# Kernel optimization log

Measured on AMD Instinct MI355X. Metric: run time of the kernel, lower is better.

Reference implementation:

```python
import jax, jax.numpy as jnp
import numpy as np

HEADS = 4

def _layernorm(x, g, b, eps=1e-5):
    mu = x.mean(-1, keepdims=True)
    var = ((x - mu) ** 2).mean(-1, keepdims=True)
    return (x - mu) / jnp.sqrt(var + eps) * g + b

def _feature_map(data, proj, is_query, eps=1e-4):
    # FAVOR+ softmax kernel features. data: [B,H,S,dh], proj: [m,dh]
    dh = data.shape[-1]
    m = proj.shape[0]
    dn = dh ** -0.25
    ratio = m ** -0.5
    dash = jnp.einsum('bhsd,md->bhsm', data * dn, proj)
    diag = 0.5 * jnp.sum((data * dn) ** 2, axis=-1, keepdims=True)
    mx = jnp.max(dash, axis=-1, keepdims=True) if is_query else jnp.max(dash)
    return ratio * (jnp.exp(dash - diag - mx) + eps)

def _causal_linear_attention(q, k, v):
    # q,k: [B,H,S,m] kernel features; v: [B,H,S,dh]
    k_cum = jnp.cumsum(k, axis=2)                                  # [B,H,S,m]
    d_inv = 1.0 / jnp.einsum('bhsm,bhsm->bhs', q, k_cum)           # [B,H,S]
    ctx = jnp.cumsum(jnp.einsum('bhsm,bhsd->bhsmd', k, v), axis=2) # [B,H,S,m,dh]
    return jnp.einsum('bhsmd,bhsm,bhs->bhsd', ctx, q, d_inv)

def reference(x, pre_w, pre_b, ln1_g, ln1_b, wq, wk, wv, wo, bo, proj,
              ln2_g, ln2_b, ff_w1, ff_b1, ff_w2, ff_b2, tgt_w, tgt_b, rd_w, rd_b):
    # preproc: 1x1x1 conv3d + softplus
    xbn = jax.nn.softplus(jnp.einsum('bcthw,oc->bothw', x, pre_w)
                          + pre_b[None, :, None, None, None])
    B, D, T, H, W = xbn.shape
    tokens = xbn.reshape(B, -1, D)  # raw torch-style reshape, S = T*H*W
    S = tokens.shape[1]

    # Performer block (depth=1): prenorm attention + prenorm FF, residuals
    h = _layernorm(tokens, ln1_g, ln1_b)
    split = lambda t: t.reshape(B, S, HEADS, -1).transpose(0, 2, 1, 3)
    q, k, v = split(h @ wq), split(h @ wk), split(h @ wv)
    qp = _feature_map(q, proj, True)
    kp = _feature_map(k, proj, False)
    attn = _causal_linear_attention(qp, kp, v)
    attn = attn.transpose(0, 2, 1, 3).reshape(B, S, D)
    tokens = tokens + attn @ wo + bo
    h2 = _layernorm(tokens, ln2_g, ln2_b)
    tokens = tokens + jax.nn.gelu(h2 @ ff_w1 + ff_b1, approximate=False) @ ff_w2 + ff_b2

    # readout
    out = tokens.reshape(B, D, T, H, W).mean(axis=2)               # [B,D,H,W]
    out = jnp.concatenate([out, x[:, 2, 0][:, None]], axis=1)      # [B,D+1,H,W]
    out = jax.lax.conv_general_dilated(out, tgt_w, (1, 1), [(2, 2), (2, 2)],
                                       dimension_numbers=('NCHW', 'OIHW', 'NCHW'))
    out = out + tgt_b[None, :, None, None]
    out = out.mean(axis=(2, 3))                                    # global avg pool -> [B,1]
    return out @ rd_w.T + rd_b


def setup_inputs() -> dict:
    key = jax.random.key(0)
    ks = jax.random.split(key, 12)
    B, T, H, W = 2, 8, 48, 48
    D, DH, M, FF = 64, 16, 32, 256
    s = lambda k, shape, sc=1.0: jax.random.normal(k, shape, jnp.float32) * sc
    inv = 1.0 / np.sqrt(D)
    return {
        'x': s(ks[0], (B, 3, T, H, W)),
        'pre_w': s(ks[1], (D, 3), 1.0 / np.sqrt(3)),
        'pre_b': jnp.zeros((D,), jnp.float32),
        'ln1_g': jnp.ones((D,), jnp.float32), 'ln1_b': jnp.zeros((D,), jnp.float32),
        'wq': s(ks[2], (D, D), inv), 'wk': s(ks[3], (D, D), inv), 'wv': s(ks[4], (D, D), inv),
        'wo': s(ks[5], (D, D), inv), 'bo': jnp.zeros((D,), jnp.float32),
        'proj': s(ks[6], (M, DH)),
        'ln2_g': jnp.ones((D,), jnp.float32), 'ln2_b': jnp.zeros((D,), jnp.float32),
        'ff_w1': s(ks[7], (D, FF), inv), 'ff_b1': jnp.zeros((FF,), jnp.float32),
        'ff_w2': s(ks[8], (FF, D), 1.0 / np.sqrt(FF)), 'ff_b2': jnp.zeros((D,), jnp.float32),
        'tgt_w': s(ks[9], (1, D + 1, 5, 5), 1.0 / np.sqrt((D + 1) * 25)),
        'tgt_b': jnp.zeros((1,), jnp.float32),
        'rd_w': s(ks[10], (1, 1)), 'rd_b': jnp.zeros((1,), jnp.float32),
    }
```

## Files before the change

### kernel.cpp

```cpp
#include <hip/hip_runtime.h>
#include <hip/hip_bf16.h>
#include <math.h>

typedef __hip_bfloat16 bf16;
typedef __attribute__((ext_vector_type(8))) short short8;
typedef __attribute__((ext_vector_type(16))) float floatx16;

constexpr int B_   = 2;
constexpr int T_   = 8;
constexpr int HW   = 48 * 48;
constexpr int S_   = T_ * HW;
constexpr int D_   = 64;
constexpr int NH   = 4;
constexpr int DH   = 16;
constexpr int M_   = 32;
constexpr int BS   = B_ * S_;
constexpr int BSD  = BS * D_;
constexpr int BH   = B_ * NH;
constexpr int BHS  = BH * S_;
constexpr int CHUNK = 32;
constexpr int NC   = S_ / CHUNK;
constexpr int STATE = M_ * DH + M_;
constexpr int GSLOTS = 64;
constexpr int GSTRIDE = 32;
constexpr int SCB = 16;
constexpr int SRG = 16;
constexpr int SRUN = NC / SRG;
constexpr float DN = 0.5f;
constexpr float RATIO = 0.17677669529663687f;

__device__ __forceinline__ unsigned short f2bf(float f) {
  bf16 h = __float2bfloat16(f);
  return *reinterpret_cast<unsigned short*>(&h);
}
__device__ __forceinline__ float bf2f(bf16 v) { return __bfloat162float(v); }
__device__ __forceinline__ float bfs2f(short s) {
  return __uint_as_float(((unsigned)(unsigned short)s) << 16);
}
__device__ __forceinline__ void atomicMaxFloat(float* addr, float val) {
  if (val >= 0.f) atomicMax((int*)addr, __float_as_int(val));
  else atomicMin((unsigned int*)addr, __float_as_uint(val));
}

__global__ void __launch_bounds__(256) k_prep(const float* __restrict__ wq,
        const float* __restrict__ wk, const float* __restrict__ wv,
        const float* __restrict__ wo, const float* __restrict__ w1,
        const float* __restrict__ proj,
        short* __restrict__ wqT, short* __restrict__ wkT, short* __restrict__ wvT,
        short* __restrict__ woT, short* __restrict__ w1T, short* __restrict__ projb,
        float* __restrict__ gmax) {
  int tid = blockIdx.x * 256 + threadIdx.x;
  if (tid < GSLOTS) ((unsigned*)gmax)[tid * GSTRIDE] = 0xff800000u;
  if (tid < 512) projb[tid] = (short)f2bf(proj[tid]);
  if (tid < 4096) {
    int c = tid >> 6, r = tid & 63;
    wqT[tid] = (short)f2bf(wq[r * 64 + c]);
    wkT[tid] = (short)f2bf(wk[r * 64 + c]);
    wvT[tid] = (short)f2bf(wv[r * 64 + c]);
    woT[tid] = (short)f2bf(wo[r * 64 + c]);
  }
  {
    int c = tid >> 6, r = tid & 63;
    w1T[tid] = (short)f2bf(w1[r * 256 + c]);
  }
}

__global__ void __launch_bounds__(256) k_preqkv(const float* __restrict__ x,
                      const float* __restrict__ pw, const float* __restrict__ pb,
                      const float* __restrict__ g, const float* __restrict__ bb,
                      const short* __restrict__ wqT, const short* __restrict__ wkT,
                      const short* __restrict__ wvT, const short* __restrict__ projb,
                      bf16* __restrict__ tok, bf16* __restrict__ q,
                      bf16* __restrict__ k, bf16* __restrict__ v,
                      float* __restrict__ gmax) {
  __shared__ __align__(16) short sh[32 * 64];
  __shared__ __align__(16) short sk[32 * 64];
  int tid = threadIdx.x;
  int tbase = blockIdx.x * 32;

  {
    size_t f0 = (size_t)tbase * 64;
    int b = (int)(f0 / ((size_t)D_ * S_));
    int rem = (int)(f0 % ((size_t)D_ * S_));
    int d = rem / S_;
    int pos0 = rem % S_;
    float w0 = pw[d * 3 + 0], w1 = pw[d * 3 + 1], w2 = pw[d * 3 + 2], pbd = pb[d];
    const float* xb = x + ((size_t)b * 3) * S_ + pos0 + tid * 8;
    float4 x0a = *(const float4*)(xb);
    float4 x0b = *(const float4*)(xb + 4);
    float4 x1a = *(const float4*)(xb + S_);
    float4 x1b = *(const float4*)(xb + S_ + 4);
    float4 x2a = *(const float4*)(xb + 2 * S_);
    float4 x2b = *(const float4*)(xb + 2 * S_ + 4);
    float xf0[8] = {x0a.x, x0a.y, x0a.z, x0a.w, x0b.x, x0b.y, x0b.z, x0b.w};
    float xf1[8] = {x1a.x, x1a.y, x1a.z, x1a.w, x1b.x, x1b.y, x1b.z, x1b.w};
    float xf2[8] = {x2a.x, x2a.y, x2a.z, x2a.w, x2b.x, x2b.y, x2b.z, x2b.w};
    float t[8];
    short8 tv;
#pragma unroll
    for (int j = 0; j < 8; ++j) {
      float a = xf0[j] * w0 + xf1[j] * w1 + xf2[j] * w2 + pbd;
      t[j] = fmaxf(a, 0.f) + log1pf(expf(-fabsf(a)));
      tv[j] = (short)f2bf(t[j]);
    }
    *(short8*)(tok + f0 + (size_t)tid * 8) = tv;
    float s1 = 0.f, s2 = 0.f;
#pragma unroll
    for (int j = 0; j < 8; ++j) { s1 += t[j]; s2 += t[j] * t[j]; }
#pragma unroll
    for (int off = 4; off; off >>= 1) {
      s1 += __shfl_xor(s1, off, 8);
      s2 += __shfl_xor(s2, off, 8);
    }
    float mu = s1 * (1.f / 64.f);
    float var = s2 * (1.f / 64.f) - mu * mu;
    float rs = rsqrtf(var + 1e-5f);
    int tt = tid >> 3, j8 = tid & 7;
    short8 hv;
#pragma unroll
    for (int j = 0; j < 8; ++j) {
      int c = j8 * 8 + j;
      hv[j] = (short)f2bf((t[j] - mu) * rs * g[c] + bb[c]);
    }
    *(short8*)&sh[tt * 64 + ((j8 ^ (tt & 7)) * 8)] = hv;
  }
  __syncthreads();

  int w = tid >> 6;
  int L = tid & 63;
  int half = L >> 5;
  int n = L & 31;

  if (w < 3) {
    const short* wmT = (w == 0) ? wqT : (w == 1) ? wkT : wvT;
    bf16* outm = (w == 0) ? q : (w == 1) ? k : v;

    short8 a[4];
#pragma unroll
    for (int c = 0; c < 4; ++c)
      a[c] = *(const short8*)&sh[n * 64 + (((c * 2 + half) ^ (n & 7)) * 8)];
#pragma unroll
    for (int ct = 0; ct < 2; ++ct) {
      int col = ct * 32 + n;
      short8 bfrag[4];
#pragma unroll
      for (int c = 0; c < 4; ++c)
        bfrag[c] = *(const short8*)&wmT[col * 64 + c * 16 + half * 8];
      floatx16 acc;
#pragma unroll
      for (int i = 0; i < 16; ++i) acc[i] = 0.f;
      acc = __builtin_amdgcn_mfma_f32_32x32x16_bf16(a[0], bfrag[0], acc, 0, 0, 0);
      acc = __builtin_amdgcn_mfma_f32_32x32x16_bf16(a[1], bfrag[1], acc, 0, 0, 0);
      acc = __builtin_amdgcn_mfma_f32_32x32x16_bf16(a[2], bfrag[2], acc, 0, 0, 0);
      acc = __builtin_amdgcn_mfma_f32_32x32x16_bf16(a[3], bfrag[3], acc, 0, 0, 0);
      int head = col >> 4, di = col & 15;
#pragma unroll
      for (int r = 0; r < 16; ++r) {
        int row = (r & 3) + 8 * (r >> 2) + 4 * half;
        int token = tbase + row;
        int b = token / S_, s = token % S_;
        unsigned short us = f2bf(acc[r]);
        if (w == 2) {
          outm[((size_t)(b * NH + head) * S_ + s) * DH + di] = *(bf16*)&us;
        } else {
          unsigned short usd = f2bf(bfs2f((short)us) * DN);
          outm[((size_t)(b * NH + head) * S_ + s) * DH + di] = *(bf16*)&usd;
          if (w == 1)
            *(short*)((char*)sk + row * 128 + ((col * 2) ^ ((row & 7) << 4))) = (short)usd;
        }
      }
    }
  }
  __syncthreads();

  {
    short8 ak;
    short8 bp = *(const short8*)&projb[n * 16 + half * 8];
    int roff = n * 128 + ((w * 32 + half * 16) ^ ((n & 7) << 4));
    ak = *(const short8*)((const char*)sk + roff);
    floatx16 Pk;
#pragma unroll
    for (int i = 0; i < 16; ++i) Pk[i] = 0.f;
    Pk = __builtin_amdgcn_mfma_f32_32x32x16_bf16(ak, bp, Pk, 0, 0, 0);
    float bmax = -3.4e38f;
#pragma unroll
    for (int r = 0; r < 16; ++r) bmax = fmaxf(bmax, Pk[r]);
    for (int off = 32; off; off >>= 1) bmax = fmaxf(bmax, __shfl_xor(bmax, off));
    if (L == 0)
      atomicMaxFloat(&gmax[((blockIdx.x * 4 + w) & (GSLOTS - 1)) * GSTRIDE], bmax);
  }
}

__global__ void __launch_bounds__(256) k_featcsfin(const float* __restrict__ gmax,
                      const bf16* __restrict__ q, const bf16* __restrict__ k,
                      const bf16* __restrict__ v, const short* __restrict__ projb,
                      bf16* __restrict__ qpb, bf16* __restrict__ kpb,
                      float* __restrict__ ckv) {
  __shared__ __align__(16) float sKp[CHUNK * 32];
  __shared__ __align__(16) float sVc[CHUNK * 16];
  int tid = threadIdx.x;
  int w = tid >> 6, L = tid & 63, half = L >> 5, n = L & 31;
  short8 bp = *(const short8*)&projb[n * 16 + half * 8];

  if (blockIdx.x >= BH * NC) {
    int fblk = blockIdx.x - BH * NC;
    int rowbase = fblk * 128 + w * 32;
    short8 aq = *(const short8*)(q + (size_t)(rowbase + n) * 16 + half * 8);
    float dq = 0.f;
#pragma unroll
    for (int j = 0; j < 8; ++j) { float f = bfs2f(aq[j]); dq += f * f; }
    dq += __shfl_xor(dq, 32);
    dq *= 0.5f;
    floatx16 Pq;
#pragma unroll
    for (int i = 0; i < 16; ++i) Pq[i] = 0.f;
    Pq = __builtin_amdgcn_mfma_f32_32x32x16_bf16(aq, bp, Pq, 0, 0, 0);
#pragma unroll
    for (int r = 0; r < 16; ++r) {
      int i = (r & 3) + 8 * (r >> 2) + 4 * half;
      float mx = Pq[r];
      for (int off = 16; off; off >>= 1) mx = fmaxf(mx, __shfl_xor(mx, off, 32));
      float dqi = __shfl(dq, i, 64);
      float val = RATIO * (expf(Pq[r] - dqi - mx) + 1e-4f);
      qpb[(size_t)(rowbase + i) * 32 + n] = __float2bfloat16(val);
    }
    return;
  }

  int blk = blockIdx.x;
  int bh = blk / NC, c = blk % NC;
  int base = bh * S_ + c * CHUNK;
  if (w == 0) {
    float gm = gmax[L * GSTRIDE];
    for (int off = 32; off; off >>= 1) gm = fmaxf(gm, __shfl_xor(gm, off));
    short8 ak = *(const short8*)(k + (size_t)(base + n) * 16 + half * 8);
    float dk = 0.f;
#pragma unroll
    for (int j = 0; j < 8; ++j) { float f = bfs2f(ak[j]); dk += f * f; }
    dk += __shfl_xor(dk, 32);
    dk *= 0.5f;
    floatx16 Pk;
#pragma unroll
    for (int i = 0; i < 16; ++i) Pk[i] = 0.f;
    Pk = __builtin_amdgcn_mfma_f32_32x32x16_bf16(ak, bp, Pk, 0, 0, 0);
#pragma unroll
    for (int r = 0; r < 16; ++r) {
      int i = (r & 3) + 8 * (r >> 2) + 4 * half;
      float dgi = __shfl(dk, i, 64);
      sKp[i * 32 + n] = RATIO * (expf(Pk[r] - dgi - gm) + 1e-4f);
    }
  } else if (w == 1) {
    int row = L >> 1, h8 = (L & 1) * 8;
    short8 vs = *(const short8*)(v + (size_t)(base + row) * 16 + h8);
#pragma unroll
    for (int j = 0; j < 8; ++j) sVc[row * 16 + h8 + j] = bfs2f(vs[j]);
  }
  __syncthreads();
  {
    int row = tid >> 3, m4 = tid & 7;
    float4 fin = *(const float4*)&sKp[row * 32 + m4 * 4];
    uint2 u;
    u.x = (unsigned)f2bf(fin.x) | ((unsigned)f2bf(fin.y) << 16);
    u.y = (unsigned)f2bf(fin.z) | ((unsigned)f2bf(fin.w) << 16);
    *(uint2*)&kpb[(size_t)(base + row) * 32 + m4 * 4] = u;
  }
  int m0 = tid >> 4, d0 = tid & 15;
  int m1 = m0 + 16;
  float a0 = 0.f, a1 = 0.f, az0 = 0.f, az1 = 0.f;
  for (int t = 0; t < CHUNK; ++t) {
    float k0 = sKp[t * 32 + m0];
    float k1 = sKp[t * 32 + m1];
    float vv = sVc[t * 16 + d0];
    a0 += k0 * vv;
    a1 += k1 * vv;
    if (d0 == 0) { az0 += k0; az1 += k1; }
  }
  float* outp = ckv + (size_t)blk * STATE;
  outp[m0 * 16 + d0] = a0;
  outp[m1 * 16 + d0] = a1;
  if (d0 == 0) { outp[512 + m0] = az0; outp[512 + m1] = az1; }
}

__global__ void __launch_bounds__(256) k_scan(float* __restrict__ ckv) {
  __shared__ float sS[SRG][SCB];
  int blk = blockIdx.x;
  int bh = blk / (STATE / SCB);
  int c0 = (blk % (STATE / SCB)) * SCB;
  int cl = threadIdx.x & (SCB - 1);
  int rg = threadIdx.x >> 4;
  int c = c0 + cl;
  size_t base = ((size_t)bh * NC + rg * SRUN) * STATE + c;
  float s = 0.f;
#pragma unroll 6
  for (int i = 0; i < SRUN; ++i) s += ckv[base + (size_t)i * STATE];
  sS[rg][cl] = s;
  __syncthreads();
  float run = 0.f;
  for (int r = 0; r < rg; ++r) run += sS[r][cl];
  for (int i0 = 0; i0 < SRUN; i0 += 6) {
    float tb[6];
#pragma unroll
    for (int j = 0; j < 6; ++j) tb[j] = ckv[base + (size_t)(i0 + j) * STATE];
#pragma unroll
    for (int j = 0; j < 6; ++j) {
      ckv[base + (size_t)(i0 + j) * STATE] = run;
      run += tb[j];
    }
  }
}

__global__ void __launch_bounds__(256) k_attn(const bf16* __restrict__ qpb,
                                              const bf16* __restrict__ kpb,
                                              const bf16* __restrict__ v,
                                              const float* __restrict__ ckv,
                                              bf16* __restrict__ attn) {
  __shared__ __align__(16) float sP[4][32 * 33 + 4];
  int tid = threadIdx.x;
  int w = tid >> 6;
  int L = tid & 63;
  int half = L >> 5;
  int n = L & 31;
  int chunk = blockIdx.x * 4 + w;
  int bh = chunk / NC, c = chunk % NC;
  int base = bh * S_ + c * CHUNK;

  short8 a1 = *(const short8*)(qpb + (size_t)(base + n) * 32 + half * 8);
  short8 a2 = *(const short8*)(qpb + (size_t)(base + n) * 32 + 16 + half * 8);
  short8 b1 = *(const short8*)(kpb + (size_t)(base + n) * 32 + half * 8);
  short8 b2 = *(const short8*)(kpb + (size_t)(base + n) * 32 + 16 + half * 8);

  floatx16 P;
#pragma unroll
  for (int i = 0; i < 16; ++i) P[i] = 0.f;
  P = __builtin_amdgcn_mfma_f32_32x32x16_bf16(a1, b1, P, 0, 0, 0);
  P = __builtin_amdgcn_mfma_f32_32x32x16_bf16(a2, b2, P, 0, 0, 0);

  float* sp = &sP[w][0];
#pragma unroll
  for (int r = 0; r < 16; ++r) {
    int i = (r & 3) + 8 * (r >> 2) + 4 * half;
    sp[i * 33 + n] = (n <= i) ? P[r] : 0.f;
  }
  __syncthreads();
  short8 pa1, pa2;
#pragma unroll
  for (int j = 0; j < 8; ++j) {
    pa1[j] = (short)f2bf(sp[n * 33 + half * 8 + j]);
    pa2[j] = (short)f2bf(sp[n * 33 + 16 + half * 8 + j]);
  }

  const float* cs = ckv + (size_t)chunk * STATE;
  const unsigned short one_bf = f2bf(1.f);
  short8 vb1, vb2, sb1, sb2;
#pragma unroll
  for (int j = 0; j < 8; ++j) {
    int t1 = half * 8 + j, t2 = 16 + half * 8 + j;
    vb1[j] = (n < 16) ? *(const short*)(v + (size_t)(base + t1) * 16 + n)
                      : (short)(n == 16 ? one_bf : 0);
    vb2[j] = (n < 16) ? *(const short*)(v + (size_t)(base + t2) * 16 + n)
                      : (short)(n == 16 ? one_bf : 0);
    float y1 = (n < 16) ? cs[t1 * 16 + n] : (n == 16 ? cs[512 + t1] : 0.f);
    float y2 = (n < 16) ? cs[t2 * 16 + n] : (n == 16 ? cs[512 + t2] : 0.f);
    sb1[j] = (short)f2bf(y1);
    sb2[j] = (short)f2bf(y2);
  }

  floatx16 O;
#pragma unroll
  for (int i = 0; i < 16; ++i) O[i] = 0.f;
  O = __builtin_amdgcn_mfma_f32_32x32x16_bf16(pa1, vb1, O, 0, 0, 0);
  O = __builtin_amdgcn_mfma_f32_32x32x16_bf16(pa2, vb2, O, 0, 0, 0);
  O = __builtin_amdgcn_mfma_f32_32x32x16_bf16(a1, sb1, O, 0, 0, 0);
  O = __builtin_amdgcn_mfma_f32_32x32x16_bf16(a2, sb2, O, 0, 0, 0);

  int srcl = 16 + 32 * half;
  float res[16];
#pragma unroll
  for (int r = 0; r < 16; ++r) {
    float den = __shfl(O[r], srcl, 64);
    res[r] = O[r] / den;
  }
  if (n < 16) {
    int b = bh >> 2, head = bh & 3;
#pragma unroll
    for (int r = 0; r < 16; ++r) {
      int i = (r & 3) + 8 * (r >> 2) + 4 * half;
      attn[((size_t)(b * S_ + c * CHUNK + i)) * 64 + head * 16 + n] = __float2bfloat16(res[r]);
    }
  }
}

__global__ void __launch_bounds__(128) k_wo_ln(const bf16* __restrict__ attn,
                        const short* __restrict__ woT, const float* __restrict__ bo,
                        const bf16* __restrict__ tok, const float* __restrict__ g,
                        const float* __restrict__ bb,
                        bf16* __restrict__ tok2, bf16* __restrict__ h2) {
  __shared__ __align__(16) float sC[32 * 68];
  int tid = threadIdx.x;
  int w = tid >> 6;
  int L = tid & 63;
  int half = L >> 5;
  int n = L & 31;
  int tbase = blockIdx.x * 32;

  short8 a[4];
  {
    const bf16* arow = attn + (size_t)(tbase + n) * 64 + half * 8;
#pragma unroll
    for (int c = 0; c < 4; ++c) a[c] = *(const short8*)(arow + c * 16);
  }
  int col = w * 32 + n;
  short8 bfrag[4];
#pragma unroll
  for (int c = 0; c < 4; ++c)
    bfrag[c] = *(const short8*)&woT[col * 64 + c * 16 + half * 8];
  floatx16 acc;
#pragma unroll
  for (int i = 0; i < 16; ++i) acc[i] = 0.f;
  acc = __builtin_amdgcn_mfma_f32_32x32x16_bf16(a[0], bfrag[0], acc, 0, 0, 0);
  acc = __builtin_amdgcn_mfma_f32_32x32x16_bf16(a[1], bfrag[1], acc, 0, 0, 0);
  acc = __builtin_amdgcn_mfma_f32_32x32x16_bf16(a[2], bfrag[2], acc, 0, 0, 0);
  acc = __builtin_amdgcn_mfma_f32_32x32x16_bf16(a[3], bfrag[3], acc, 0, 0, 0);
  float bias = bo[col];
#pragma unroll
  for (int r = 0; r < 16; ++r) {
    int row = (r & 3) + 8 * (r >> 2) + 4 * half;
    sC[row * 68 + col] = acc[r] + bf2f(tok[(size_t)(tbase + row) * 64 + col]) + bias;
  }
  __syncthreads();
  int tg = tid >> 5, cg = tid & 31;
  int c0 = cg * 2, c1 = c0 + 1;
  float g0 = g[c0], g1 = g[c1], be0 = bb[c0], be1 = bb[c1];
#pragma unroll
  for (int i = 0; i < 8; ++i) {
    int lrow = tg * 8 + i;
    int token = tbase + lrow;
    float t0 = sC[lrow * 68 + c0];
    float t1 = sC[lrow * 68 + c1];
    float s1 = t0 + t1, s2 = t0 * t0 + t1 * t1;
    for (int off = 16; off; off >>= 1) {
      s1 += __shfl_xor(s1, off, 32);
      s2 += __shfl_xor(s2, off, 32);
    }
    float mu = s1 * (1.f / 64.f);
    float var = s2 * (1.f / 64.f) - mu * mu;
    float rs = rsqrtf(var + 1e-5f);
    tok2[token * 64 + c0] = __float2bfloat16(t0);
    tok2[token * 64 + c1] = __float2bfloat16(t1);
    h2[token * 64 + c0] = __float2bfloat16((t0 - mu) * rs * g0 + be0);
    h2[token * 64 + c1] = __float2bfloat16((t1 - mu) * rs * g1 + be1);
  }
}

__global__ void __launch_bounds__(256) k_ffg(const bf16* __restrict__ h2,
                                             const short* __restrict__ w1T,
                                             const float* __restrict__ b1,
                                             float* __restrict__ Gavg) {
  int tid = threadIdx.x;
  int w = tid >> 6;
  int L = tid & 63;
  int half = L >> 5;
  int n = L & 31;
  int blk = blockIdx.x;
  int b = blk / 576;
  int rem = blk % 576;
  int ch = rem / 9;
  int jp0 = (rem % 9) * 4;
  int token_n = b * 18432 + ch * 288 + (n & 7) * 36 + jp0 + (n >> 3);

  short8 a[4];
  {
    const bf16* hrow = h2 + (size_t)token_n * 64 + half * 8;
#pragma unroll
    for (int c = 0; c < 4; ++c) a[c] = *(const short8*)(hrow + c * 16);
  }
  size_t gbase = ((size_t)(b * 64 + ch) * 36 + jp0);
#pragma unroll
  for (int ct = 0; ct < 2; ++ct) {
    int col = w * 64 + ct * 32 + n;
    short8 bfrag[4];
#pragma unroll
    for (int c = 0; c < 4; ++c)
      bfrag[c] = *(const short8*)&w1T[col * 64 + c * 16 + half * 8];
    floatx16 acc;
#pragma unroll
    for (int i = 0; i < 16; ++i) acc[i] = 0.f;
    acc = __builtin_amdgcn_mfma_f32_32x32x16_bf16(a[0], bfrag[0], acc, 0, 0, 0);
    acc = __builtin_amdgcn_mfma_f32_32x32x16_bf16(a[1], bfrag[1], acc, 0, 0, 0);
    acc = __builtin_amdgcn_mfma_f32_32x32x16_bf16(a[2], bfrag[2], acc, 0, 0, 0);
    acc = __builtin_amdgcn_mfma_f32_32x32x16_bf16(a[3], bfrag[3], acc, 0, 0, 0);
    float bias = b1[col];
#pragma unroll
    for (int j = 0; j < 4; ++j) {
      float s = 0.f;
#pragma unroll
      for (int rr = 0; rr < 4; ++rr) {
        float xg = acc[j * 4 + rr] + bias;
        s += 0.5f * xg * (1.f + erff(xg * 0.70710678118654752f));
      }
      s += __shfl_xor(s, 32);
      if (half == 0)
        Gavg[(gbase + j) * 256 + col] = s * 0.125f;
    }
  }
}

__global__ void __launch_bounds__(256) k_pool2(const float* __restrict__ Gavg,
                        const bf16* __restrict__ tok2, const float* __restrict__ w2,
                        const float* __restrict__ b2, float* __restrict__ pool) {
  __shared__ __align__(16) float sG[18 * 256];
  __shared__ __align__(16) float sRed[4 * 18 * 64];
  int blk = blockIdx.x;
  int b = blk / 128;
  int rem = blk % 128;
  int ch = rem >> 1, jph = rem & 1;
  int tid = threadIdx.x;
  size_t grow0 = ((size_t)(b * 64 + ch) * 36 + jph * 18) * 256;
  for (int e = tid; e < 1152; e += 256) {
    int row = e >> 6, c4 = e & 63;
    *(float4*)&sG[row * 256 + c4 * 4] = *(const float4*)&Gavg[grow0 + row * 256 + c4 * 4];
  }
  __syncthreads();
  int kg = tid >> 6, dd = tid & 63;
  float acc[18];
#pragma unroll
  for (int i = 0; i < 18; ++i) acc[i] = 0.f;
  for (int k4 = 0; k4 < 16; ++k4) {
    int k = kg * 64 + k4 * 4;
    float w0 = w2[(k + 0) * 64 + dd];
    float w1 = w2[(k + 1) * 64 + dd];
    float w2v = w2[(k + 2) * 64 + dd];
    float w3 = w2[(k + 3) * 64 + dd];
#pragma unroll
    for (int i = 0; i < 18; ++i) {
      float4 gf = *(const float4*)&sG[i * 256 + k];
      acc[i] += gf.x * w0 + gf.y * w1 + gf.z * w2v + gf.w * w3;
    }
  }
#pragma unroll
  for (int i = 0; i < 18; ++i) sRed[(kg * 18 + i) * 64 + dd] = acc[i];
  __syncthreads();
  for (int o = tid; o < 1152; o += 256) {
    int jp18 = o >> 6, d2 = o & 63;
    float gsum = sRed[(0 * 18 + jp18) * 64 + d2] + sRed[(1 * 18 + jp18) * 64 + d2]
               + sRed[(2 * 18 + jp18) * 64 + d2] + sRed[(3 * 18 + jp18) * 64 + d2];
    int p = (jph * 18 + jp18) * 64 + d2;
    size_t tbase = (size_t)b * 1179648 + (size_t)ch * 18432 + p;
    float ts = 0.f;
#pragma unroll
    for (int t = 0; t < 8; ++t) ts += bf2f(tok2[tbase + t * 2304]);
    pool[((size_t)(b * 64 + ch)) * HW + p] = ts * 0.125f + gsum + b2[d2];
  }
}

__global__ void __launch_bounds__(256) k_convsum(const float* __restrict__ pool,
                                                 const float* __restrict__ x,
                                                 const float* __restrict__ w,
                                                 float* __restrict__ partial) {
  int blk = blockIdx.x;
  int b = blk / 65, ch = blk % 65;
  int tid = threadIdx.x;
  __shared__ float cls[25];
  __shared__ float red[256];
  if (tid < 25) {
    int ry = tid / 5, rx = tid % 5;
    int kh0 = (ry <= 2) ? 0 : (ry == 3 ? 1 : 2);
    int kh1 = (ry >= 2) ? 4 : (ry == 1 ? 3 : 2);
    int kw0 = (rx <= 2) ? 0 : (rx == 3 ? 1 : 2);
    int kw1 = (rx >= 2) ? 4 : (rx == 1 ? 3 : 2);
    float s = 0.f;
    for (int kh = kh0; kh <= kh1; ++kh)
      for (int kw = kw0; kw <= kw1; ++kw)
        s += w[ch * 25 + kh * 5 + kw];
    cls[tid] = s;
  }
  __syncthreads();
  const float* pc = (ch < 64) ? (pool + ((size_t)(b * 64 + ch)) * HW)
                              : (x + (size_t)b * 3 * S_ + 2 * S_);
  float acc = 0.f;
#pragma unroll
  for (int e = tid; e < HW; e += 256) {
    int iy = e / 48, ix = e % 48;
    int ry = (iy == 0) ? 0 : (iy == 1) ? 1 : (iy <= 45) ? 2 : (iy == 46) ? 3 : 4;
    int rx = (ix == 0) ? 0 : (ix == 1) ? 1 : (ix <= 45) ? 2 : (ix == 46) ? 3 : 4;
    acc += pc[e] * cls[ry * 5 + rx];
  }
  red[tid] = acc;
  __syncthreads();
  for (int s = 128; s; s >>= 1) {
    if (tid < s) red[tid] += red[tid + s];
    __syncthreads();
  }
  if (!tid) partial[blk] = red[0];
}

__global__ void k_final(const float* __restrict__ partial, const float* __restrict__ tgt_b,
                        const float* __restrict__ rd_w, const float* __restrict__ rd_b,
                        float* __restrict__ out) {
  int b = blockIdx.x;
  int lane = threadIdx.x;
  float s = (lane < 65) ? partial[b * 65 + lane] : 0.f;
  for (int off = 32; off; off >>= 1) s += __shfl_down(s, off, 64);
  __shared__ float r2;
  if (lane == 64) r2 = s;
  __syncthreads();
  if (!lane) {
    float tot = s + r2;
    float mean = tot / 2304.f + tgt_b[0];
    out[b] = mean * rd_w[0] + rd_b[0];
  }
}

extern "C" void kernel_launch(void* const* d_in, const int* in_sizes, int n_in,
                              void* d_out, int out_size, void* d_ws, size_t ws_size,
                              hipStream_t stream) {
  const float* x     = (const float*)d_in[0];
  const float* pre_w = (const float*)d_in[1];
  const float* pre_b = (const float*)d_in[2];
  const float* ln1_g = (const float*)d_in[3];
  const float* ln1_b = (const float*)d_in[4];
  const float* wq    = (const float*)d_in[5];
  const float* wk    = (const float*)d_in[6];
  const float* wv    = (const float*)d_in[7];
  const float* wo    = (const float*)d_in[8];
  const float* bo    = (const float*)d_in[9];
  const float* proj  = (const float*)d_in[10];
  const float* ln2_g = (const float*)d_in[11];
  const float* ln2_b = (const float*)d_in[12];
  const float* ff_w1 = (const float*)d_in[13];
  const float* ff_b1 = (const float*)d_in[14];
  const float* ff_w2 = (const float*)d_in[15];
  const float* ff_b2 = (const float*)d_in[16];
  const float* tgt_w = (const float*)d_in[17];
  const float* tgt_b = (const float*)d_in[18];
  const float* rd_w  = (const float*)d_in[19];
  const float* rd_b  = (const float*)d_in[20];
  float* out = (float*)d_out;

  float* ws = (float*)d_ws;
  bf16*  tok   = (bf16*)ws;
  bf16*  v     = (bf16*)(ws + (size_t)BSD);
  bf16*  q     = (bf16*)(ws + 2 * (size_t)BSD);
  float* Gavg  = ws + 2 * (size_t)BSD;
  float* pool  = Gavg + 1179648;
  bf16*  k     = (bf16*)(ws + 3 * (size_t)BSD);
  bf16*  h2    = (bf16*)(ws + 4 * (size_t)BSD);
  bf16*  qpb   = (bf16*)(ws + 6 * (size_t)BSD);
  bf16*  kpb   = (bf16*)(ws + 7 * (size_t)BSD);
  float* ckv   = ws + 8 * (size_t)BSD;
  bf16*  tok2  = (bf16*)(ws + 8 * (size_t)BSD);
  bf16*  attnb = k;
  float* smalls = ws + 9 * (size_t)BSD + 147456;
  float* gmax  = smalls;
  float* partial = smalls + 2048;
  short* wqT   = (short*)(smalls + 2304);
  short* wkT   = (short*)(smalls + 4352);
  short* wvT   = (short*)(smalls + 6400);
  short* woT   = (short*)(smalls + 8448);
  short* w1T   = (short*)(smalls + 10496);
  short* projb = (short*)(smalls + 18688);

  k_prep<<<dim3(64), dim3(256), 0, stream>>>(wq, wk, wv, wo, ff_w1, proj,
                                             wqT, wkT, wvT, woT, w1T, projb, gmax);
  k_preqkv<<<dim3(BS / 32), dim3(256), 0, stream>>>(x, pre_w, pre_b, ln1_g, ln1_b,
                                                    wqT, wkT, wvT, projb, tok, q, k, v, gmax);
  k_featcsfin<<<dim3(BH * NC + BHS / 128), dim3(256), 0, stream>>>(gmax, q, k, v, projb,
                                                                   qpb, kpb, ckv);
  k_scan<<<dim3(BH * (STATE / SCB)), dim3(256), 0, stream>>>(ckv);
  k_attn<<<dim3(BH * NC / 4), dim3(256), 0, stream>>>(qpb, kpb, v, ckv, attnb);
  k_wo_ln<<<dim3(BS / 32), dim3(128), 0, stream>>>(attnb, woT, bo, tok, ln2_g, ln2_b, tok2, h2);
  k_ffg<<<dim3(B_ * 64 * 9), dim3(256), 0, stream>>>(h2, w1T, ff_b1, Gavg);
  k_pool2<<<dim3(B_ * 64 * 2), dim3(256), 0, stream>>>(Gavg, tok2, ff_w2, ff_b2, pool);
  k_convsum<<<dim3(B_ * 65), dim3(256), 0, stream>>>(pool, x, tgt_w, partial);
  k_final<<<dim3(B_), dim3(128), 0, stream>>>(partial, tgt_b, rd_w, rd_b, out);
}
```

Measured before the change: 206.7 us.

## Compute per-chunk KV state with MFMA, one chunk per wavefront

The chunk-state kernel now gives each of the four wavefronts in a block its own chunk instead of one chunk per 256-thread block. The per-chunk K^T·V outer-product sum and the K column sum are done with two bf16 MFMA instructions, using a ones column appended to V, instead of a scalar loop over LDS. The block-wide __syncthreads is removed and the grid shrinks fourfold. In exchange, the state is accumulated from bf16-rounded kernel features rather than fp32 ones, which slightly lowers precision. V is read with scalar 2-byte loads that are gathered per lane.

Measured after the change: 195.3 us. 5.5% less time.

```diff
diff --git a/kernel.cpp b/kernel.cpp
--- a/kernel.cpp
+++ b/kernel.cpp
@@ -196,14 +196,13 @@
                       const bf16* __restrict__ v, const short* __restrict__ projb,
                       bf16* __restrict__ qpb, bf16* __restrict__ kpb,
                       float* __restrict__ ckv) {
-  __shared__ __align__(16) float sKp[CHUNK * 32];
-  __shared__ __align__(16) float sVc[CHUNK * 16];
+  __shared__ __align__(16) float sKp[4][CHUNK * 32];
   int tid = threadIdx.x;
   int w = tid >> 6, L = tid & 63, half = L >> 5, n = L & 31;
   short8 bp = *(const short8*)&projb[n * 16 + half * 8];
 
-  if (blockIdx.x >= BH * NC) {
-    int fblk = blockIdx.x - BH * NC;
+  if (blockIdx.x >= BH * NC / 4) {
+    int fblk = blockIdx.x - BH * NC / 4;
     int rowbase = fblk * 128 + w * 32;
     short8 aq = *(const short8*)(q + (size_t)(rowbase + n) * 16 + half * 8);
     float dq = 0.f;
@@ -227,58 +226,71 @@
     return;
   }
 
-  int blk = blockIdx.x;
-  int bh = blk / NC, c = blk % NC;
+  int chunk = blockIdx.x * 4 + w;
+  int bh = chunk / NC, c = chunk % NC;
   int base = bh * S_ + c * CHUNK;
-  if (w == 0) {
-    float gm = gmax[L * GSTRIDE];
-    for (int off = 32; off; off >>= 1) gm = fmaxf(gm, __shfl_xor(gm, off));
-    short8 ak = *(const short8*)(k + (size_t)(base + n) * 16 + half * 8);
-    float dk = 0.f;
-#pragma unroll
-    for (int j = 0; j < 8; ++j) { float f = bfs2f(ak[j]); dk += f * f; }
-    dk += __shfl_xor(dk, 32);
-    dk *= 0.5f;
-    floatx16 Pk;
-#pragma unroll
-    for (int i = 0; i < 16; ++i) Pk[i] = 0.f;
-    Pk = __builtin_amdgcn_mfma_f32_32x32x16_bf16(ak, bp, Pk, 0, 0, 0);
-#pragma unroll
-    for (int r = 0; r < 16; ++r) {
-      int i = (r & 3) + 8 * (r >> 2) + 4 * half;
-      float dgi = __shfl(dk, i, 64);
-      sKp[i * 32 + n] = RATIO * (expf(Pk[r] - dgi - gm) + 1e-4f);
-    }
-  } else if (w == 1) {
-    int row = L >> 1, h8 = (L & 1) * 8;
-    short8 vs = *(const short8*)(v + (size_t)(base + row) * 16 + h8);
-#pragma unroll
-    for (int j = 0; j < 8; ++j) sVc[row * 16 + h8 + j] = bfs2f(vs[j]);
-  }
-  __syncthreads();
+  float gm = gmax[L * GSTRIDE];
+  for (int off = 32; off; off >>= 1) gm = fmaxf(gm, __shfl_xor(gm, off));
+  short8 ak = *(const short8*)(k + (size_t)(base + n) * 16 + half * 8);
+  float dk = 0.f;
+#pragma unroll
+  for (int j = 0; j < 8; ++j) { float f = bfs2f(ak[j]); dk += f * f; }
+  dk += __shfl_xor(dk, 32);
+  dk *= 0.5f;
+  floatx16 Pk;
+#pragma unroll
+  for (int i = 0; i < 16; ++i) Pk[i] = 0.f;
+  Pk = __builtin_amdgcn_mfma_f32_32x32x16_bf16(ak, bp, Pk, 0, 0, 0);
+  float* sp = &sKp[w][0];
+#pragma unroll
+  for (int r = 0; r < 16; ++r) {
+    int i = (r & 3) + 8 * (r >> 2) + 4 * half;
+    float dgi = __shfl(dk, i, 64);
+    sp[i * 32 + n] = RATIO * (expf(Pk[r] - dgi - gm) + 1e-4f);
+  }
+  short8 a1, a2;
+#pragma unroll
+  for (int j = 0; j < 8; ++j) {
+    a1[j] = (short)f2bf(sp[(half * 8 + j) * 32 + n]);
+    a2[j] = (short)f2bf(sp[(16 + half * 8 + j) * 32 + n]);
+  }
+  const unsigned short one_bf = f2bf(1.f);
+  short8 vb1, vb2;
+#pragma unroll
+  for (int j = 0; j < 8; ++j) {
+    int t1 = half * 8 + j, t2 = 16 + half * 8 + j;
+    vb1[j] = (n < 16) ? *(const short*)(v + (size_t)(base + t1) * 16 + n)
+                      : (short)(n == 16 ? one_bf : 0);
+    vb2[j] = (n < 16) ? *(const short*)(v + (size_t)(base + t2) * 16 + n)
+                      : (short)(n == 16 ? one_bf : 0);
+  }
+  floatx16 O;
+#pragma unroll
+  for (int i = 0; i < 16; ++i) O[i] = 0.f;
+  O = __builtin_amdgcn_mfma_f32_32x32x16_bf16(a1, vb1, O, 0, 0, 0);
+  O = __builtin_amdgcn_mfma_f32_32x32x16_bf16(a2, vb2, O, 0, 0, 0);
+  float* outp = ckv + (size_t)chunk * STATE;
+#pragma unroll
+  for (int r = 0; r < 16; ++r) {
+    int m = (r & 3) + 8 * (r >> 2) + 4 * half;
+    if (n < 16) outp[m * 16 + n] = O[r];
+    else if (n == 16) outp[512 + m] = O[r];
+  }
   {
-    int row = tid >> 3, m4 = tid & 7;
-    float4 fin = *(const float4*)&sKp[row * 32 + m4 * 4];
-    uint2 u;
-    u.x = (unsigned)f2bf(fin.x) | ((unsigned)f2bf(fin.y) << 16);
-    u.y = (unsigned)f2bf(fin.z) | ((unsigned)f2bf(fin.w) << 16);
-    *(uint2*)&kpb[(size_t)(base + row) * 32 + m4 * 4] = u;
-  }
-  int m0 = tid >> 4, d0 = tid & 15;
-  int m1 = m0 + 16;
-  float a0 = 0.f, a1 = 0.f, az0 = 0.f, az1 = 0.f;
-  for (int t = 0; t < CHUNK; ++t) {
-    float k0 = sKp[t * 32 + m0];
-    float k1 = sKp[t * 32 + m1];
-    float vv = sVc[t * 16 + d0];
-    a0 += k0 * vv;
-    a1 += k1 * vv;
-    if (d0 == 0) { az0 += k0; az1 += k1; }
-  }
-  float* outp = ckv + (size_t)blk * STATE;
-  outp[m0 * 16 + d0] = a0;
-  outp[m1 * 16 + d0] = a1;
-  if (d0 == 0) { outp[512 + m0] = az0; outp[512 + m1] = az1; }
+    int row = L >> 1, c8 = (L & 1) * 16;
+    const float* srcp = sp + row * 32 + c8;
+    uint4 u0, u1;
+    u0.x = (unsigned)f2bf(srcp[0])  | ((unsigned)f2bf(srcp[1])  << 16);
+    u0.y = (unsigned)f2bf(srcp[2])  | ((unsigned)f2bf(srcp[3])  << 16);
+    u0.z = (unsigned)f2bf(srcp[4])  | ((unsigned)f2bf(srcp[5])  << 16);
+    u0.w = (unsigned)f2bf(srcp[6])  | ((unsigned)f2bf(srcp[7])  << 16);
+    u1.x = (unsigned)f2bf(srcp[8])  | ((unsigned)f2bf(srcp[9])  << 16);
+    u1.y = (unsigned)f2bf(srcp[10]) | ((unsigned)f2bf(srcp[11]) << 16);
+    u1.z = (unsigned)f2bf(srcp[12]) | ((unsigned)f2bf(srcp[13]) << 16);
+    u1.w = (unsigned)f2bf(srcp[14]) | ((unsigned)f2bf(srcp[15]) << 16);
+    *(uint4*)&kpb[(size_t)(base + row) * 32 + c8] = u0;
+    *(uint4*)&kpb[(size_t)(base + row) * 32 + c8 + 8] = u1;
+  }
 }
 
 __global__ void __launch_bounds__(256) k_scan(float* __restrict__ ckv) {
@@ -664,8 +676,8 @@
                                              wqT, wkT, wvT, woT, w1T, projb, gmax);
   k_preqkv<<<dim3(BS / 32), dim3(256), 0, stream>>>(x, pre_w, pre_b, ln1_g, ln1_b,
                                                     wqT, wkT, wvT, projb, tok, q, k, v, gmax);
-  k_featcsfin<<<dim3(BH * NC + BHS / 128), dim3(256), 0, stream>>>(gmax, q, k, v, projb,
-                                                                   qpb, kpb, ckv);
+  k_featcsfin<<<dim3(BH * NC / 4 + BHS / 128), dim3(256), 0, stream>>>(gmax, q, k, v, projb,
+                                                                       qpb, kpb, ckv);
   k_scan<<<dim3(BH * (STATE / SCB)), dim3(256), 0, stream>>>(ckv);
   k_attn<<<dim3(BH * NC / 4), dim3(256), 0, stream>>>(qpb, kpb, v, ckv, attnb);
   k_wo_ln<<<dim3(BS / 32), dim3(128), 0, stream>>>(attnb, woT, bo, tok, ln2_g, ln2_b, tok2, h2);
```
